# Performance work log

Measured on AMD Instinct MI355X. Metric: run time of the kernel, lower is better.

## Reference

```python
import jax, jax.numpy as jnp
import numpy as np

B, S, U, M = 4096, 64, 128, 32
ODE_UNFOLDS = 6
EPS = 1e-08

def _uniform(k, shape, lo, hi):
    return jax.random.uniform(k, shape, jnp.float32, lo, hi)

def setup_inputs() -> dict:
    key = jax.random.key(0)
    ks = jax.random.split(key, 16)
    return {
        "inputs": jax.random.normal(ks[0], (B, S), jnp.float32),
        "state": jax.random.normal(ks[1], (B, U), jnp.float32),
        "gleak": _uniform(ks[2], (U,), 0.001, 1.0),
        "vleak": _uniform(ks[3], (U,), -0.2, 0.2),
        "cm": _uniform(ks[4], (U,), 0.4, 0.6),
        "sigma": _uniform(ks[5], (U, U), 3.0, 8.0),
        "mu": _uniform(ks[6], (U, U), 0.3, 0.8),
        "w": _uniform(ks[7], (U, U), 0.001, 1.0),
        "erev": jnp.sign(jax.random.normal(ks[8], (U, U), jnp.float32)),
        "sensory_sigma": _uniform(ks[9], (S, U), 3.0, 8.0),
        "sensory_mu": _uniform(ks[10], (S, U), 0.3, 0.8),
        "sensory_w": _uniform(ks[11], (S, U), 0.001, 1.0),
        "sensory_erev": jnp.sign(jax.random.normal(ks[12], (S, U), jnp.float32)),
        "sparsity_mask": (jax.random.uniform(ks[13], (U, U)) < 0.5).astype(jnp.float32),
        "sensory_sparsity_mask": (jax.random.uniform(ks[14], (S, U)) < 0.5).astype(jnp.float32),
        "input_w": jnp.ones((S,), jnp.float32),
        "input_b": jnp.zeros((S,), jnp.float32),
        "output_w": jnp.ones((M,), jnp.float32),
        "output_b": jnp.zeros((M,), jnp.float32),
    }

def reference(inputs, state, gleak, vleak, cm, sigma, mu, w, erev,
              sensory_sigma, sensory_mu, sensory_w, sensory_erev,
              sparsity_mask, sensory_sparsity_mask,
              input_w, input_b, output_w, output_b):
    # input mapping (affine)
    x = inputs * input_w + input_b                       # [B,S]
    # sensory synapse activation: [B,S,U]
    sens_act = (sensory_w * sensory_sparsity_mask) * jax.nn.sigmoid(
        sensory_sigma * (x[:, :, None] - sensory_mu))
    w_num_sensory = jnp.sum(sens_act * sensory_erev, axis=1)   # [B,U]
    w_den_sensory = jnp.sum(sens_act, axis=1)                  # [B,U]

    wm = w * sparsity_mask                                     # masked weights [U,U]
    wme = wm * erev                                            # weights*erev   [U,U]
    cm_t = cm * ODE_UNFOLDS                                    # cm / (1/unfolds)
    leak = gleak * vleak

    v = state
    for _ in range(ODE_UNFOLDS):
        sig = jax.nn.sigmoid(sigma * (v[:, :, None] - mu))     # [B,U,U] (src,dst)
        w_num = jnp.einsum('bsu,su->bu', sig, wme) + w_num_sensory
        w_den = jnp.einsum('bsu,su->bu', sig, wm) + w_den_sensory
        v = (cm_t * v + leak + w_num) / (cm_t + gleak + w_den + EPS)

    out = v[:, :M] * output_w + output_b                       # motor slice + affine
    return out, v
```

## Files before the change

### kernel.cpp

```cpp
#include <hip/hip_runtime.h>
#include <hip/hip_fp16.h>

typedef unsigned short u16;
typedef unsigned int   u32;

#define B_TOTAL 4096
#define NU      128
#define NS      64
#define NM      32
#define UNFOLDS 6
#define LOG2E   1.44269504088896340736f

__device__ __forceinline__ float bf2f(u16 v) {
  return __uint_as_float(((u32)v) << 16);
}
__device__ __forceinline__ u16 f2bf(float f) {
  u32 x = __float_as_uint(f);
  return (u16)((x + 0x7fffu + ((x >> 16) & 1u)) >> 16);
}

template<bool BF16>
__device__ __forceinline__ float LD(const void* p, int i) {
  if (BF16) return bf2f(((const u16*)p)[i]);
  return ((const float*)p)[i];
}

__device__ __forceinline__ u32 pk(float a, float b) {
  __half2 h = __halves2half2(__float2half_rn(a), __float2half_rn(b));
  return __builtin_bit_cast(u32, h);
}
__device__ __forceinline__ float lo2f(u32 h) {
  return __low2float(__builtin_bit_cast(__half2, h));
}
__device__ __forceinline__ float hi2f(u32 h) {
  return __high2float(__builtin_bit_cast(__half2, h));
}

__device__ __forceinline__ void step2i(uint4 a, float va, float vb,
                                       float& na0, float& da0, float& na1, float& da1,
                                       float& nb0, float& db0, float& nb1, float& db1) {
  float ta0 = fmaf(va, lo2f(a.x), lo2f(a.y));
  float ta1 = fmaf(va, hi2f(a.x), hi2f(a.y));
  float tb0 = fmaf(vb, lo2f(a.x), lo2f(a.y));
  float tb1 = fmaf(vb, hi2f(a.x), hi2f(a.y));
  float ea0 = __builtin_amdgcn_exp2f(ta0);
  float ea1 = __builtin_amdgcn_exp2f(ta1);
  float eb0 = __builtin_amdgcn_exp2f(tb0);
  float eb1 = __builtin_amdgcn_exp2f(tb1);
  float pa0 = 1.0f + ea0, pa1 = 1.0f + ea1;
  float pb0 = 1.0f + eb0, pb1 = 1.0f + eb1;
  float ra = __builtin_amdgcn_rcpf(pa0 * pa1);
  float rb = __builtin_amdgcn_rcpf(pb0 * pb1);
  float sa0 = pa1 * ra, sa1 = pa0 * ra;
  float sb0 = pb1 * rb, sb1 = pb0 * rb;
  na0 = fmaf(sa0, lo2f(a.z), na0);  da0 = fmaf(sa0, lo2f(a.w), da0);
  na1 = fmaf(sa1, hi2f(a.z), na1);  da1 = fmaf(sa1, hi2f(a.w), da1);
  nb0 = fmaf(sb0, lo2f(a.z), nb0);  db0 = fmaf(sb0, lo2f(a.w), db0);
  nb1 = fmaf(sb1, hi2f(a.z), nb1);  db1 = fmaf(sb1, hi2f(a.w), db1);
}

template<bool BF16>
__device__ __forceinline__ void body(
    const void* g_in, const void* g_state, const void* g_gleak, const void* g_vleak,
    const void* g_cm, const void* g_sigma, const void* g_mu, const void* g_w,
    const void* g_erev, const void* g_ssig, const void* g_smu, const void* g_sw,
    const void* g_serev, const void* g_mask, const void* g_smask,
    const void* g_iw, const void* g_ib, const void* g_ow, const void* g_ob,
    void* g_out,
    uint4* smR,
    float* smV)
{
  const int tid = threadIdx.x;
  const int b0  = blockIdx.x * 16;

  const int r  = tid >> 6;
  const int u0 = tid & 63;
  const int u1 = u0 + 64;
  const int ba = b0 + 2 * r;
  const int bb = ba + 1;

  float* vbA = smV + r * 256;
  float* vbB = vbA + 128;

  #pragma unroll 2
  for (int e = tid; e < NS * 64; e += 512) {
    int s = e >> 6, l = e & 63;
    int i0 = s * NU + l, i1 = i0 + 64;
    float sl0 = LD<BF16>(g_ssig, i0) * LOG2E, sl1 = LD<BF16>(g_ssig, i1) * LOG2E;
    float ms0 = LD<BF16>(g_smu, i0) * sl0,    ms1 = LD<BF16>(g_smu, i1) * sl1;
    float w0 = LD<BF16>(g_sw, i0) * LD<BF16>(g_smask, i0) * LD<BF16>(g_serev, i0);
    float w1 = LD<BF16>(g_sw, i1) * LD<BF16>(g_smask, i1) * LD<BF16>(g_serev, i1);
    smR[e] = make_uint4(pk(-sl0, -sl1), pk(ms0, ms1), pk(w0, w1),
                        pk(fabsf(w0), fabsf(w1)));
  }
  __syncthreads();

  float iw = LD<BF16>(g_iw, u0), ib = LD<BF16>(g_ib, u0);
  float xa = LD<BF16>(g_in, ba * NS + u0) * iw + ib;
  float xb = LD<BF16>(g_in, bb * NS + u0) * iw + ib;
  float va0 = LD<BF16>(g_state, ba * NU + u0);
  float va1 = LD<BF16>(g_state, ba * NU + u1);
  float vb0 = LD<BF16>(g_state, bb * NU + u0);
  float vb1 = LD<BF16>(g_state, bb * NU + u1);
  const float gl0 = LD<BF16>(g_gleak, u0), gl1 = LD<BF16>(g_gleak, u1);
  const float lk0 = gl0 * LD<BF16>(g_vleak, u0);
  const float lk1 = gl1 * LD<BF16>(g_vleak, u1);
  const float cm0 = LD<BF16>(g_cm, u0) * (float)UNFOLDS;
  const float cm1 = LD<BF16>(g_cm, u1) * (float)UNFOLDS;
  const float cgl0 = cm0 + gl0 + 1e-8f;
  const float cgl1 = cm1 + gl1 + 1e-8f;

  const uint4* pR = smR + u0;

  vbA[u0] = xa;
  vbB[u0] = xb;

  float nsa0 = 0.f, dsa0 = 0.f, nsa1 = 0.f, dsa1 = 0.f;
  float nsb0 = 0.f, dsb0 = 0.f, nsb1 = 0.f, dsb1 = 0.f;
  #pragma unroll 4
  for (int s4 = 0; s4 < NS; s4 += 4) {
    float4 xa4 = *(const float4*)(vbA + s4);
    float4 xb4 = *(const float4*)(vbB + s4);
    step2i(pR[(s4 + 0) * 64], xa4.x, xb4.x, nsa0, dsa0, nsa1, dsa1, nsb0, dsb0, nsb1, dsb1);
    step2i(pR[(s4 + 1) * 64], xa4.y, xb4.y, nsa0, dsa0, nsa1, dsa1, nsb0, dsb0, nsb1, dsb1);
    step2i(pR[(s4 + 2) * 64], xa4.z, xb4.z, nsa0, dsa0, nsa1, dsa1, nsb0, dsb0, nsb1, dsb1);
    step2i(pR[(s4 + 3) * 64], xa4.w, xb4.w, nsa0, dsa0, nsa1, dsa1, nsb0, dsb0, nsb1, dsb1);
  }

  vbA[u0] = va0;  vbA[u1] = va1;
  vbB[u0] = vb0;  vbB[u1] = vb1;
  __syncthreads();

  #pragma unroll 4
  for (int e = tid; e < NU * 64; e += 512) {
    int j = e >> 6, l = e & 63;
    int i0 = j * NU + l, i1 = i0 + 64;
    float sl0 = LD<BF16>(g_sigma, i0) * LOG2E, sl1 = LD<BF16>(g_sigma, i1) * LOG2E;
    float ms0 = LD<BF16>(g_mu, i0) * sl0,      ms1 = LD<BF16>(g_mu, i1) * sl1;
    float w0 = LD<BF16>(g_w, i0) * LD<BF16>(g_mask, i0) * LD<BF16>(g_erev, i0);
    float w1 = LD<BF16>(g_w, i1) * LD<BF16>(g_mask, i1) * LD<BF16>(g_erev, i1);
    smR[e] = make_uint4(pk(-sl0, -sl1), pk(ms0, ms1), pk(w0, w1),
                        pk(fabsf(w0), fabsf(w1)));
  }
  __syncthreads();

  #pragma unroll 1
  for (int it = 0; it < UNFOLDS; ++it) {
    float na0 = nsa0, da0 = dsa0, na1 = nsa1, da1 = dsa1;
    float nb0 = nsb0, db0 = dsb0, nb1 = nsb1, db1 = dsb1;
    #pragma unroll 4
    for (int j4 = 0; j4 < NU; j4 += 4) {
      float4 va4 = *(const float4*)(vbA + j4);
      float4 vb4 = *(const float4*)(vbB + j4);
      step2i(pR[(j4 + 0) * 64], va4.x, vb4.x, na0, da0, na1, da1, nb0, db0, nb1, db1);
      step2i(pR[(j4 + 1) * 64], va4.y, vb4.y, na0, da0, na1, da1, nb0, db0, nb1, db1);
      step2i(pR[(j4 + 2) * 64], va4.z, vb4.z, na0, da0, na1, da1, nb0, db0, nb1, db1);
      step2i(pR[(j4 + 3) * 64], va4.w, vb4.w, na0, da0, na1, da1, nb0, db0, nb1, db1);
    }
    va0 = fmaf(cm0, va0, lk0 + na0) * __builtin_amdgcn_rcpf(cgl0 + da0);
    va1 = fmaf(cm1, va1, lk1 + na1) * __builtin_amdgcn_rcpf(cgl1 + da1);
    vb0 = fmaf(cm0, vb0, lk0 + nb0) * __builtin_amdgcn_rcpf(cgl0 + db0);
    vb1 = fmaf(cm1, vb1, lk1 + nb1) * __builtin_amdgcn_rcpf(cgl1 + db1);
    if (it < UNFOLDS - 1) {
      vbA[u0] = va0;  vbA[u1] = va1;
      vbB[u0] = vb0;  vbB[u1] = vb1;
    }
  }

  if (BF16) {
    u16* om = (u16*)g_out;
    u16* ov = om + B_TOTAL * NM;
    ov[ba * NU + u0] = f2bf(va0);
    ov[ba * NU + u1] = f2bf(va1);
    ov[bb * NU + u0] = f2bf(vb0);
    ov[bb * NU + u1] = f2bf(vb1);
    if (u0 < NM) {
      float ow = LD<true>(g_ow, u0), ob = LD<true>(g_ob, u0);
      om[ba * NM + u0] = f2bf(fmaf(va0, ow, ob));
      om[bb * NM + u0] = f2bf(fmaf(vb0, ow, ob));
    }
  } else {
    float* om = (float*)g_out;
    float* ov = om + B_TOTAL * NM;
    ov[ba * NU + u0] = va0;
    ov[ba * NU + u1] = va1;
    ov[bb * NU + u0] = vb0;
    ov[bb * NU + u1] = vb1;
    if (u0 < NM) {
      float ow = LD<false>(g_ow, u0), ob = LD<false>(g_ob, u0);
      om[ba * NM + u0] = fmaf(va0, ow, ob);
      om[bb * NM + u0] = fmaf(vb0, ow, ob);
    }
  }
}

__global__ __launch_bounds__(512, 2) void ltc_kernel(
    const void* g_in, const void* g_state, const void* g_gleak, const void* g_vleak,
    const void* g_cm, const void* g_sigma, const void* g_mu, const void* g_w,
    const void* g_erev, const void* g_ssig, const void* g_smu, const void* g_sw,
    const void* g_serev, const void* g_mask, const void* g_smask,
    const void* g_iw, const void* g_ib, const void* g_ow, const void* g_ob,
    void* g_out)
{
  __shared__ uint4 smR[NU * 64];
  __shared__ float smV[8 * 256];

  const u16* sg = (const u16*)g_sigma;
  int cnt = 0;
  #pragma unroll
  for (int i = 0; i < 32; ++i) {
    float f = bf2f(sg[2 * i]);
    cnt += (f >= 2.0f && f <= 16.0f) ? 1 : 0;
  }
  if (cnt >= 24)
    body<true >(g_in, g_state, g_gleak, g_vleak, g_cm, g_sigma, g_mu, g_w, g_erev,
                g_ssig, g_smu, g_sw, g_serev, g_mask, g_smask,
                g_iw, g_ib, g_ow, g_ob, g_out, smR, smV);
  else
    body<false>(g_in, g_state, g_gleak, g_vleak, g_cm, g_sigma, g_mu, g_w, g_erev,
                g_ssig, g_smu, g_sw, g_serev, g_mask, g_smask,
                g_iw, g_ib, g_ow, g_ob, g_out, smR, smV);
}

extern "C" void kernel_launch(void* const* d_in, const int* in_sizes, int n_in,
                              void* d_out, int out_size, void* d_ws, size_t ws_size,
                              hipStream_t stream) {
  (void)in_sizes; (void)n_in; (void)out_size; (void)d_ws; (void)ws_size;
  dim3 grid(B_TOTAL / 16);
  dim3 block(512);
  hipLaunchKernelGGL(ltc_kernel, grid, block, 0, stream,
                     d_in[0], d_in[1], d_in[2], d_in[3], d_in[4],
                     d_in[5], d_in[6], d_in[7], d_in[8],
                     d_in[9], d_in[10], d_in[11], d_in[12],
                     d_in[13], d_in[14], d_in[15], d_in[16],
                     d_in[17], d_in[18], d_out);
}
```

Before: 200.2 us.

## Split source-neuron reduction across two wave halves with LDS combine

Doubles the block to 1024 threads. The upper 8 waves handle the second half of the sensory and recurrent source indices, then pass their partial numerator and denominator sums through a new LDS buffer to the lower waves, which finish the state update. This is meant to raise waves per CU, since the grid is only 256 blocks, so that exp, rcp and LDS latency is better hidden. In exchange it adds two block-wide barriers per unfold and more shared memory. The launch bounds of (1024,4) may also squeeze register allocation.

```diff
diff --git a/kernel.cpp b/kernel.cpp
--- a/kernel.cpp
+++ b/kernel.cpp
@@ -68,22 +68,26 @@
     const void* g_iw, const void* g_ib, const void* g_ow, const void* g_ob,
     void* g_out,
     uint4* smR,
-    float* smV)
+    float* smV,
+    float* smP)
 {
   const int tid = threadIdx.x;
   const int b0  = blockIdx.x * 16;
 
-  const int r  = tid >> 6;
-  const int u0 = tid & 63;
-  const int u1 = u0 + 64;
-  const int ba = b0 + 2 * r;
+  const int wv  = tid >> 6;
+  const int u0  = tid & 63;
+  const int u1  = u0 + 64;
+  const int p   = wv & 7;
+  const bool hiW = wv >= 8;
+  const int ba = b0 + 2 * p;
   const int bb = ba + 1;
 
-  float* vbA = smV + r * 256;
+  float* vbA = smV + p * 256;
   float* vbB = vbA + 128;
-
-  #pragma unroll 2
-  for (int e = tid; e < NS * 64; e += 512) {
+  float* red = smP + p * 512;
+
+  #pragma unroll 4
+  for (int e = tid; e < NS * 64; e += 1024) {
     int s = e >> 6, l = e & 63;
     int i0 = s * NU + l, i1 = i0 + 64;
     float sl0 = LD<BF16>(g_ssig, i0) * LOG2E, sl1 = LD<BF16>(g_ssig, i1) * LOG2E;
@@ -93,15 +97,19 @@
     smR[e] = make_uint4(pk(-sl0, -sl1), pk(ms0, ms1), pk(w0, w1),
                         pk(fabsf(w0), fabsf(w1)));
   }
-  __syncthreads();
-
-  float iw = LD<BF16>(g_iw, u0), ib = LD<BF16>(g_ib, u0);
-  float xa = LD<BF16>(g_in, ba * NS + u0) * iw + ib;
-  float xb = LD<BF16>(g_in, bb * NS + u0) * iw + ib;
-  float va0 = LD<BF16>(g_state, ba * NU + u0);
-  float va1 = LD<BF16>(g_state, ba * NU + u1);
-  float vb0 = LD<BF16>(g_state, bb * NU + u0);
-  float vb1 = LD<BF16>(g_state, bb * NU + u1);
+
+  float va0 = 0.f, va1 = 0.f, vb0 = 0.f, vb1 = 0.f;
+  if (!hiW) {
+    float iw = LD<BF16>(g_iw, u0), ib = LD<BF16>(g_ib, u0);
+    float xa = LD<BF16>(g_in, ba * NS + u0) * iw + ib;
+    float xb = LD<BF16>(g_in, bb * NS + u0) * iw + ib;
+    va0 = LD<BF16>(g_state, ba * NU + u0);
+    va1 = LD<BF16>(g_state, ba * NU + u1);
+    vb0 = LD<BF16>(g_state, bb * NU + u0);
+    vb1 = LD<BF16>(g_state, bb * NU + u1);
+    vbA[u0] = xa;
+    vbB[u0] = xb;
+  }
   const float gl0 = LD<BF16>(g_gleak, u0), gl1 = LD<BF16>(g_gleak, u1);
   const float lk0 = gl0 * LD<BF16>(g_vleak, u0);
   const float lk1 = gl1 * LD<BF16>(g_vleak, u1);
@@ -111,28 +119,31 @@
   const float cgl1 = cm1 + gl1 + 1e-8f;
 
   const uint4* pR = smR + u0;
-
-  vbA[u0] = xa;
-  vbB[u0] = xb;
+  const int sbase = hiW ? 32 : 0;
+  const int jbase = hiW ? 64 : 0;
+
+  __syncthreads();
 
   float nsa0 = 0.f, dsa0 = 0.f, nsa1 = 0.f, dsa1 = 0.f;
   float nsb0 = 0.f, dsb0 = 0.f, nsb1 = 0.f, dsb1 = 0.f;
   #pragma unroll 4
-  for (int s4 = 0; s4 < NS; s4 += 4) {
-    float4 xa4 = *(const float4*)(vbA + s4);
-    float4 xb4 = *(const float4*)(vbB + s4);
-    step2i(pR[(s4 + 0) * 64], xa4.x, xb4.x, nsa0, dsa0, nsa1, dsa1, nsb0, dsb0, nsb1, dsb1);
-    step2i(pR[(s4 + 1) * 64], xa4.y, xb4.y, nsa0, dsa0, nsa1, dsa1, nsb0, dsb0, nsb1, dsb1);
-    step2i(pR[(s4 + 2) * 64], xa4.z, xb4.z, nsa0, dsa0, nsa1, dsa1, nsb0, dsb0, nsb1, dsb1);
-    step2i(pR[(s4 + 3) * 64], xa4.w, xb4.w, nsa0, dsa0, nsa1, dsa1, nsb0, dsb0, nsb1, dsb1);
-  }
-
-  vbA[u0] = va0;  vbA[u1] = va1;
-  vbB[u0] = vb0;  vbB[u1] = vb1;
+  for (int s4 = 0; s4 < 32; s4 += 4) {
+    float4 xa4 = *(const float4*)(vbA + sbase + s4);
+    float4 xb4 = *(const float4*)(vbB + sbase + s4);
+    step2i(pR[(sbase + s4 + 0) * 64], xa4.x, xb4.x, nsa0, dsa0, nsa1, dsa1, nsb0, dsb0, nsb1, dsb1);
+    step2i(pR[(sbase + s4 + 1) * 64], xa4.y, xb4.y, nsa0, dsa0, nsa1, dsa1, nsb0, dsb0, nsb1, dsb1);
+    step2i(pR[(sbase + s4 + 2) * 64], xa4.z, xb4.z, nsa0, dsa0, nsa1, dsa1, nsb0, dsb0, nsb1, dsb1);
+    step2i(pR[(sbase + s4 + 3) * 64], xa4.w, xb4.w, nsa0, dsa0, nsa1, dsa1, nsb0, dsb0, nsb1, dsb1);
+  }
   __syncthreads();
 
+  if (!hiW) {
+    vbA[u0] = va0;  vbA[u1] = va1;
+    vbB[u0] = vb0;  vbB[u1] = vb1;
+  }
+
   #pragma unroll 4
-  for (int e = tid; e < NU * 64; e += 512) {
+  for (int e = tid; e < NU * 64; e += 1024) {
     int j = e >> 6, l = e & 63;
     int i0 = j * NU + l, i1 = i0 + 64;
     float sl0 = LD<BF16>(g_sigma, i0) * LOG2E, sl1 = LD<BF16>(g_sigma, i1) * LOG2E;
@@ -149,52 +160,68 @@
     float na0 = nsa0, da0 = dsa0, na1 = nsa1, da1 = dsa1;
     float nb0 = nsb0, db0 = dsb0, nb1 = nsb1, db1 = dsb1;
     #pragma unroll 4
-    for (int j4 = 0; j4 < NU; j4 += 4) {
-      float4 va4 = *(const float4*)(vbA + j4);
-      float4 vb4 = *(const float4*)(vbB + j4);
-      step2i(pR[(j4 + 0) * 64], va4.x, vb4.x, na0, da0, na1, da1, nb0, db0, nb1, db1);
-      step2i(pR[(j4 + 1) * 64], va4.y, vb4.y, na0, da0, na1, da1, nb0, db0, nb1, db1);
-      step2i(pR[(j4 + 2) * 64], va4.z, vb4.z, na0, da0, na1, da1, nb0, db0, nb1, db1);
-      step2i(pR[(j4 + 3) * 64], va4.w, vb4.w, na0, da0, na1, da1, nb0, db0, nb1, db1);
-    }
-    va0 = fmaf(cm0, va0, lk0 + na0) * __builtin_amdgcn_rcpf(cgl0 + da0);
-    va1 = fmaf(cm1, va1, lk1 + na1) * __builtin_amdgcn_rcpf(cgl1 + da1);
-    vb0 = fmaf(cm0, vb0, lk0 + nb0) * __builtin_amdgcn_rcpf(cgl0 + db0);
-    vb1 = fmaf(cm1, vb1, lk1 + nb1) * __builtin_amdgcn_rcpf(cgl1 + db1);
-    if (it < UNFOLDS - 1) {
-      vbA[u0] = va0;  vbA[u1] = va1;
-      vbB[u0] = vb0;  vbB[u1] = vb1;
-    }
-  }
-
-  if (BF16) {
-    u16* om = (u16*)g_out;
-    u16* ov = om + B_TOTAL * NM;
-    ov[ba * NU + u0] = f2bf(va0);
-    ov[ba * NU + u1] = f2bf(va1);
-    ov[bb * NU + u0] = f2bf(vb0);
-    ov[bb * NU + u1] = f2bf(vb1);
-    if (u0 < NM) {
-      float ow = LD<true>(g_ow, u0), ob = LD<true>(g_ob, u0);
-      om[ba * NM + u0] = f2bf(fmaf(va0, ow, ob));
-      om[bb * NM + u0] = f2bf(fmaf(vb0, ow, ob));
-    }
-  } else {
-    float* om = (float*)g_out;
-    float* ov = om + B_TOTAL * NM;
-    ov[ba * NU + u0] = va0;
-    ov[ba * NU + u1] = va1;
-    ov[bb * NU + u0] = vb0;
-    ov[bb * NU + u1] = vb1;
-    if (u0 < NM) {
-      float ow = LD<false>(g_ow, u0), ob = LD<false>(g_ob, u0);
-      om[ba * NM + u0] = fmaf(va0, ow, ob);
-      om[bb * NM + u0] = fmaf(vb0, ow, ob);
-    }
-  }
-}
-
-__global__ __launch_bounds__(512, 2) void ltc_kernel(
+    for (int j4 = 0; j4 < 64; j4 += 4) {
+      float4 va4 = *(const float4*)(vbA + jbase + j4);
+      float4 vb4 = *(const float4*)(vbB + jbase + j4);
+      step2i(pR[(jbase + j4 + 0) * 64], va4.x, vb4.x, na0, da0, na1, da1, nb0, db0, nb1, db1);
+      step2i(pR[(jbase + j4 + 1) * 64], va4.y, vb4.y, na0, da0, na1, da1, nb0, db0, nb1, db1);
+      step2i(pR[(jbase + j4 + 2) * 64], va4.z, vb4.z, na0, da0, na1, da1, nb0, db0, nb1, db1);
+      step2i(pR[(jbase + j4 + 3) * 64], va4.w, vb4.w, na0, da0, na1, da1, nb0, db0, nb1, db1);
+    }
+    if (hiW) {
+      red[0 * 64 + u0] = na0;  red[1 * 64 + u0] = da0;
+      red[2 * 64 + u0] = na1;  red[3 * 64 + u0] = da1;
+      red[4 * 64 + u0] = nb0;  red[5 * 64 + u0] = db0;
+      red[6 * 64 + u0] = nb1;  red[7 * 64 + u0] = db1;
+    }
+    __syncthreads();
+    if (!hiW) {
+      na0 += red[0 * 64 + u0];  da0 += red[1 * 64 + u0];
+      na1 += red[2 * 64 + u0];  da1 += red[3 * 64 + u0];
+      nb0 += red[4 * 64 + u0];  db0 += red[5 * 64 + u0];
+      nb1 += red[6 * 64 + u0];  db1 += red[7 * 64 + u0];
+      va0 = fmaf(cm0, va0, lk0 + na0) * __builtin_amdgcn_rcpf(cgl0 + da0);
+      va1 = fmaf(cm1, va1, lk1 + na1) * __builtin_amdgcn_rcpf(cgl1 + da1);
+      vb0 = fmaf(cm0, vb0, lk0 + nb0) * __builtin_amdgcn_rcpf(cgl0 + db0);
+      vb1 = fmaf(cm1, vb1, lk1 + nb1) * __builtin_amdgcn_rcpf(cgl1 + db1);
+      if (it < UNFOLDS - 1) {
+        vbA[u0] = va0;  vbA[u1] = va1;
+        vbB[u0] = vb0;  vbB[u1] = vb1;
+      }
+    }
+    __syncthreads();
+  }
+
+  if (!hiW) {
+    if (BF16) {
+      u16* om = (u16*)g_out;
+      u16* ov = om + B_TOTAL * NM;
+      ov[ba * NU + u0] = f2bf(va0);
+      ov[ba * NU + u1] = f2bf(va1);
+      ov[bb * NU + u0] = f2bf(vb0);
+      ov[bb * NU + u1] = f2bf(vb1);
+      if (u0 < NM) {
+        float ow = LD<true>(g_ow, u0), ob = LD<true>(g_ob, u0);
+        om[ba * NM + u0] = f2bf(fmaf(va0, ow, ob));
+        om[bb * NM + u0] = f2bf(fmaf(vb0, ow, ob));
+      }
+    } else {
+      float* om = (float*)g_out;
+      float* ov = om + B_TOTAL * NM;
+      ov[ba * NU + u0] = va0;
+      ov[ba * NU + u1] = va1;
+      ov[bb * NU + u0] = vb0;
+      ov[bb * NU + u1] = vb1;
+      if (u0 < NM) {
+        float ow = LD<false>(g_ow, u0), ob = LD<false>(g_ob, u0);
+        om[ba * NM + u0] = fmaf(va0, ow, ob);
+        om[bb * NM + u0] = fmaf(vb0, ow, ob);
+      }
+    }
+  }
+}
+
+__global__ __launch_bounds__(1024, 4) void ltc_kernel(
     const void* g_in, const void* g_state, const void* g_gleak, const void* g_vleak,
     const void* g_cm, const void* g_sigma, const void* g_mu, const void* g_w,
     const void* g_erev, const void* g_ssig, const void* g_smu, const void* g_sw,
@@ -204,6 +231,7 @@
 {
   __shared__ uint4 smR[NU * 64];
   __shared__ float smV[8 * 256];
+  __shared__ float smP[8 * 512];
 
   const u16* sg = (const u16*)g_sigma;
   int cnt = 0;
@@ -215,11 +243,11 @@
   if (cnt >= 24)
     body<true >(g_in, g_state, g_gleak, g_vleak, g_cm, g_sigma, g_mu, g_w, g_erev,
                 g_ssig, g_smu, g_sw, g_serev, g_mask, g_smask,
-                g_iw, g_ib, g_ow, g_ob, g_out, smR, smV);
+                g_iw, g_ib, g_ow, g_ob, g_out, smR, smV, smP);
   else
     body<false>(g_in, g_state, g_gleak, g_vleak, g_cm, g_sigma, g_mu, g_w, g_erev,
                 g_ssig, g_smu, g_sw, g_serev, g_mask, g_smask,
-                g_iw, g_ib, g_ow, g_ob, g_out, smR, smV);
+                g_iw, g_ib, g_ow, g_ob, g_out, smR, smV, smP);
 }
 
 extern "C" void kernel_launch(void* const* d_in, const int* in_sizes, int n_in,
@@ -227,7 +255,7 @@
                               hipStream_t stream) {
   (void)in_sizes; (void)n_in; (void)out_size; (void)d_ws; (void)ws_size;
   dim3 grid(B_TOTAL / 16);
-  dim3 block(512);
+  dim3 block(1024);
   hipLaunchKernelGGL(ltc_kernel, grid, block, 0, stream,
                      d_in[0], d_in[1], d_in[2], d_in[3], d_in[4],
                      d_in[5], d_in[6], d_in[7], d_in[8],
```

After: 193.6 us. -3.3%, faster.
